# Kernel tuning notes

Measured on AMD Instinct MI355X. Metric: run time of the kernel, lower is better.

Reference implementation:

```python
import jax, jax.numpy as jnp
import numpy as np

N, E, IN, H, L, NB, G = 50000, 300000, 64, 256, 4, 181, 64
EPS = 1e-5
NEG_SLOPE = 0.2


def segment_softmax(e, seg, n):
    m = jax.ops.segment_max(e, seg, num_segments=n)
    a = jnp.exp(e - m[seg])
    d = jax.ops.segment_sum(a, seg, num_segments=n)
    return a / d[seg]


def setup_inputs() -> dict:
    key = jax.random.key(0)
    ks = jax.random.split(key, 32)
    p = lambda k, shape, fan: (jax.random.normal(k, shape, jnp.float32) / np.sqrt(fan)).astype(jnp.float32)
    inp = {}
    inp["x"] = jax.random.normal(ks[0], (N, IN), jnp.float32)
    inp["edge_index"] = jax.random.randint(ks[1], (2, E), 0, N, jnp.int64)
    inp["batch"] = jnp.sort(jax.random.randint(ks[2], (N,), 0, G, jnp.int64))
    inp["W_in"] = p(ks[3], (H, IN), IN); inp["b_in"] = jnp.zeros((H,), jnp.float32)
    inp["Wl"] = p(ks[4], (L, H, H), H); inp["bl"] = jnp.zeros((L, H), jnp.float32)
    inp["Wr"] = p(ks[5], (L, H, H), H); inp["br"] = jnp.zeros((L, H), jnp.float32)
    inp["att"] = p(ks[6], (L, H), H)
    inp["bias_c"] = jnp.zeros((L, H), jnp.float32)
    inp["ln_g"] = jnp.ones((L, H), jnp.float32); inp["ln_b"] = jnp.zeros((L, H), jnp.float32)
    inp["Wg1"] = p(ks[7], (H, H), H); inp["bg1"] = jnp.zeros((H,), jnp.float32)
    inp["Wg2"] = p(ks[8], (1, H), H); inp["bg2"] = jnp.zeros((1,), jnp.float32)
    inp["Ws"] = p(ks[9], (H, H), H); inp["bs"] = jnp.zeros((H,), jnp.float32)
    inp["Wc"] = p(ks[10], (NB, H), H); inp["bc"] = jnp.zeros((NB,), jnp.float32)
    inp["Wr1"] = p(ks[11], (128, H), H); inp["br1"] = jnp.zeros((128,), jnp.float32)
    inp["Wr2"] = p(ks[12], (1, 128), 128); inp["br2"] = jnp.zeros((1,), jnp.float32)
    return inp


def reference(x, edge_index, batch, W_in, b_in, Wl, bl, Wr, br, att, bias_c, ln_g, ln_b,
              Wg1, bg1, Wg2, bg2, Ws, bs, Wc, bc, Wr1, br1, Wr2, br2):
    n = x.shape[0]
    x = x @ W_in.T + b_in  # input projection -> [N,H]
    loops = jnp.arange(n)
    src = jnp.concatenate([edge_index[0], loops])  # GATv2 add_self_loops=True
    dst = jnp.concatenate([edge_index[1], loops])
    for l in range(L):
        x_res = x
        xl = x @ Wl[l].T + bl[l]  # lin_l (source)
        xr = x @ Wr[l].T + br[l]  # lin_r (target)
        h = jax.nn.leaky_relu(xl[src] + xr[dst], NEG_SLOPE)  # [E+N, H]
        e = h @ att[l]                                       # [E+N]
        alpha = segment_softmax(e, dst, n)
        out = jax.ops.segment_sum(alpha[:, None] * xl[src], dst, num_segments=n) + bias_c[l]
        mu = out.mean(-1, keepdims=True)
        var = out.var(-1, keepdims=True)
        out = (out - mu) / jnp.sqrt(var + EPS) * ln_g[l] + ln_b[l]
        x = jax.nn.relu(out) + x_res  # dropout is identity at eval
    gate = jax.nn.relu(x @ Wg1.T + bg1) @ Wg2.T + bg2  # [N,1]
    a = segment_softmax(gate[:, 0], batch, G)
    pooled = jax.ops.segment_sum(a[:, None] * x, batch, num_segments=G)  # [G,H]
    z = jax.nn.relu(pooled @ Ws.T + bs)
    cls_logits = z @ Wc.T + bc                                   # [G,NB]
    residual = jnp.tanh(jax.nn.relu(z @ Wr1.T + br1) @ Wr2.T + br2)[:, 0]  # [G]
    return cls_logits, residual
```

## Files before the change

### kernel.cpp

```cpp
#include <hip/hip_runtime.h>
#include <math.h>

#define N_NODES 50000
#define N_EDGES 300000
#define IN_DIM 64
#define H 256
#define LAYERS 4
#define NB 181
#define NGRAPH 64
#define EE (N_EDGES + N_NODES)
#define NEG_SLOPE 0.2f
#define LN_EPS 1e-5f

typedef unsigned short u16;
typedef __attribute__((ext_vector_type(8))) _Float16 half8;
typedef __attribute__((ext_vector_type(2))) _Float16 half2v;
typedef __attribute__((ext_vector_type(4))) float floatx4;

__device__ __forceinline__ u16 f2h(float f) {
  _Float16 h = (_Float16)f;
  return __builtin_bit_cast(u16, h);
}
__device__ __forceinline__ float h2f(u16 b) {
  return (float)__builtin_bit_cast(_Float16, b);
}

__device__ __forceinline__ float wave_reduce_sum(float v) {
  #pragma unroll
  for (int off = 32; off > 0; off >>= 1) v += __shfl_xor(v, off, 64);
  return v;
}

__global__ void cast_f16_kernel(const float* __restrict__ in, u16* __restrict__ out, int n4) {
  int i = blockIdx.x * 256 + threadIdx.x;
  if (i < n4) {
    float4 f = ((const float4*)in)[i];
    ushort4 o;
    o.x = f2h(f.x); o.y = f2h(f.y); o.z = f2h(f.z); o.w = f2h(f.w);
    ((ushort4*)out)[i] = o;
  }
}

__global__ void cast_weights_kernel(
    const float* __restrict__ W_in, const float* __restrict__ Wg1,
    const float* __restrict__ Wl, const float* __restrict__ Wr,
    u16* __restrict__ win_h, u16* __restrict__ wg1_h,
    u16* __restrict__ wl_h, u16* __restrict__ wr_h)
{
  int i = blockIdx.x * 256 + threadIdx.x;
  int which = blockIdx.y;
  const float* s; u16* dd; int n4;
  if (which == 0)      { s = W_in; dd = win_h; n4 = H * IN_DIM / 4; }
  else if (which == 1) { s = Wg1;  dd = wg1_h; n4 = H * H / 4; }
  else if (which == 2) { s = Wl;   dd = wl_h;  n4 = LAYERS * H * H / 4; }
  else                 { s = Wr;   dd = wr_h;  n4 = LAYERS * H * H / 4; }
  if (i < n4) {
    float4 f = ((const float4*)s)[i];
    ushort4 o;
    o.x = f2h(f.x); o.y = f2h(f.y); o.z = f2h(f.z); o.w = f2h(f.w);
    ((ushort4*)dd)[i] = o;
  }
}

__global__ void init_counts_kernel(int* __restrict__ cnt) {
  int i = blockIdx.x * 256 + threadIdx.x;
  if (i < N_NODES) cnt[i] = 1;
}

__global__ void count_edges_kernel(const int* __restrict__ dst, int* __restrict__ cnt) {
  int e = blockIdx.x * 256 + threadIdx.x;
  if (e < N_EDGES) atomicAdd(&cnt[dst[e]], 1);
}

__global__ void scan_blocks_kernel(const int* __restrict__ cnt, int* __restrict__ partial,
                                   int* __restrict__ bsums, int n) {
  __shared__ int buf[256];
  int tid = threadIdx.x;
  int i = blockIdx.x * 256 + tid;
  buf[tid] = (i < n) ? cnt[i] : 0;
  __syncthreads();
  #pragma unroll
  for (int off = 1; off < 256; off <<= 1) {
    int t = (tid >= off) ? buf[tid - off] : 0;
    __syncthreads();
    buf[tid] += t;
    __syncthreads();
  }
  if (i < n) partial[i] = buf[tid];
  if (tid == 255) bsums[blockIdx.x] = buf[255];
}

__global__ void scan_sums_kernel(int* __restrict__ bsums, int nblk) {
  __shared__ int buf[256];
  int tid = threadIdx.x;
  buf[tid] = (tid < nblk) ? bsums[tid] : 0;
  __syncthreads();
  #pragma unroll
  for (int off = 1; off < 256; off <<= 1) {
    int t = (tid >= off) ? buf[tid - off] : 0;
    __syncthreads();
    buf[tid] += t;
    __syncthreads();
  }
  if (tid < nblk) bsums[tid] = buf[tid];
}

__global__ void scan_write_kernel(const int* __restrict__ partial, const int* __restrict__ bsums,
                                  int* __restrict__ rowp, int n) {
  int i = blockIdx.x * 256 + threadIdx.x;
  if (i < n) {
    int b = blockIdx.x;
    int off = (b > 0) ? bsums[b - 1] : 0;
    rowp[i + 1] = partial[i] + off;
    if (i == 0) rowp[0] = 0;
  }
}

__global__ void fill_self_kernel(const int* __restrict__ rowp, int* __restrict__ col,
                                 int* __restrict__ fillpos) {
  int i = blockIdx.x * 256 + threadIdx.x;
  if (i < N_NODES) {
    int p = rowp[i];
    col[p] = i;
    fillpos[i] = p + 1;
  }
}

__global__ void fill_edges_kernel(const int* __restrict__ src, const int* __restrict__ dst,
                                  int* __restrict__ fillpos, int* __restrict__ col) {
  int e = blockIdx.x * 256 + threadIdx.x;
  if (e < N_EDGES) {
    int d = dst[e];
    int p = atomicAdd(&fillpos[d], 1);
    col[p] = src[e];
  }
}

#define GTM 128
#define GTK 64
#define LDB 72
#define SSTR 132

__global__ __launch_bounds__(256) void gemm_proj_kernel(
    const u16* __restrict__ A, const u16* __restrict__ W,
    const float* __restrict__ bias, u16* __restrict__ outh, int M, int K)
{
  __shared__ u16 smem[2 * GTM * LDB];
  u16* As = smem;
  u16* Bs = smem + GTM * LDB;
  int tid = threadIdx.x;
  int lane = tid & 63;
  int wave = tid >> 6;
  int wm = (wave >> 1) * 64;
  int wn = (wave & 1) * 64;
  int bm = blockIdx.y * GTM;
  int n0 = blockIdx.x * 128;
  int lr = tid >> 3;
  int lc = (tid & 7) * 8;

  floatx4 zero4 = {0.f, 0.f, 0.f, 0.f};
  floatx4 acc[4][4];
  #pragma unroll
  for (int i = 0; i < 4; i++)
    #pragma unroll
    for (int j = 0; j < 4; j++) acc[i][j] = zero4;

  int q8 = (lane >> 4) * 8;
  int mrow = lane & 15;

  for (int k0 = 0; k0 < K; k0 += GTK) {
    __syncthreads();
    #pragma unroll
    for (int p = 0; p < 4; p++) {
      int row = lr + p * 32;
      int gr = bm + row;
      uint4 av = {0, 0, 0, 0};
      if (gr < M) av = *(const uint4*)&A[(size_t)gr * K + k0 + lc];
      *(uint4*)&As[row * LDB + lc] = av;
      uint4 bv = *(const uint4*)&W[(size_t)(n0 + row) * K + k0 + lc];
      *(uint4*)&Bs[row * LDB + lc] = bv;
    }
    __syncthreads();
    #pragma unroll
    for (int h = 0; h < 2; h++) {
      half8 af[4], bf[4];
      #pragma unroll
      for (int i = 0; i < 4; i++)
        af[i] = *(const half8*)&As[(wm + i * 16 + mrow) * LDB + h * 32 + q8];
      #pragma unroll
      for (int j = 0; j < 4; j++)
        bf[j] = *(const half8*)&Bs[(wn + j * 16 + mrow) * LDB + h * 32 + q8];
      #pragma unroll
      for (int i = 0; i < 4; i++)
        #pragma unroll
        for (int j = 0; j < 4; j++)
          acc[i][j] = __builtin_amdgcn_mfma_f32_16x16x32_f16(af[i], bf[j], acc[i][j], 0, 0, 0);
    }
  }

  __syncthreads();
  u16* stage = smem;
  int ccol = lane & 15;
  int crow4 = (lane >> 4) * 4;
  #pragma unroll
  for (int j = 0; j < 4; j++) {
    float bv = bias[n0 + wn + j * 16 + ccol];
    #pragma unroll
    for (int i = 0; i < 4; i++) {
      #pragma unroll
      for (int r = 0; r < 4; r++) {
        int row = wm + i * 16 + crow4 + r;
        stage[row * SSTR + wn + j * 16 + ccol] = f2h(acc[i][j][r] + bv);
      }
    }
  }
  __syncthreads();
  int rr = tid >> 1;
  int c0 = (tid & 1) * 64;
  int grow = bm + rr;
  if (grow < M) {
    const ushort4* sp = (const ushort4*)&stage[rr * SSTR + c0];
    ushort4* gp = (ushort4*)&outh[(size_t)grow * H + n0 + c0];
    #pragma unroll
    for (int q = 0; q < 16; q++) gp[q] = sp[q];
  }
}

#define DTM 64
#define AST 264
#define SSTR2 132

__global__ __launch_bounds__(256) void gemm_dual2_kernel(
    const u16* __restrict__ A, const u16* __restrict__ Wlb, const u16* __restrict__ Wrb,
    const float* __restrict__ biasL, const float* __restrict__ biasR,
    u16* __restrict__ outL, u16* __restrict__ outR, int M)
{
  __shared__ u16 As[DTM * AST];
  __shared__ u16 Bs[128 * LDB];
  int tid = threadIdx.x;
  int lane = tid & 63;
  int wave = tid >> 6;
  int wn = wave * 32;
  int bm = blockIdx.x * DTM;
  int mrow = lane & 15;
  int q8 = (lane >> 4) * 8;
  int ccol = lane & 15;
  int crow4 = (lane >> 4) * 4;

  {
    int col = (tid & 31) * 8;
    int r0 = tid >> 5;
    #pragma unroll
    for (int it = 0; it < 8; it++) {
      int row = r0 + it * 8;
      int gr = bm + row;
      uint4 av = {0, 0, 0, 0};
      if (gr < M) av = *(const uint4*)&A[(size_t)gr * H + col];
      *(uint4*)&As[row * AST + col] = av;
    }
  }

  floatx4 zero4 = {0.f, 0.f, 0.f, 0.f};

  for (int nt = 0; nt < 4; nt++) {
    const u16* W = (nt < 2) ? Wlb : Wrb;
    const float* bias = (nt < 2) ? biasL : biasR;
    u16* outp = (nt < 2) ? outL : outR;
    int n0 = (nt & 1) * 128;

    floatx4 acc[4][2];
    #pragma unroll
    for (int i = 0; i < 4; i++) {
      acc[i][0] = zero4;
      acc[i][1] = zero4;
    }

    for (int k0 = 0; k0 < H; k0 += 64) {
      __syncthreads();
      {
        int col = (tid & 7) * 8;
        int r0 = tid >> 3;
        #pragma unroll
        for (int p2 = 0; p2 < 4; p2++) {
          int row = r0 + p2 * 32;
          uint4 bv = *(const uint4*)&W[(size_t)(n0 + row) * H + k0 + col];
          *(uint4*)&Bs[row * LDB + col] = bv;
        }
      }
      __syncthreads();
      #pragma unroll
      for (int h = 0; h < 2; h++) {
        half8 af[4], bf[2];
        #pragma unroll
        for (int i = 0; i < 4; i++)
          af[i] = *(const half8*)&As[(i * 16 + mrow) * AST + k0 + h * 32 + q8];
        #pragma unroll
        for (int j = 0; j < 2; j++)
          bf[j] = *(const half8*)&Bs[(wn + j * 16 + mrow) * LDB + h * 32 + q8];
        #pragma unroll
        for (int i = 0; i < 4; i++)
          #pragma unroll
          for (int j = 0; j < 2; j++)
            acc[i][j] = __builtin_amdgcn_mfma_f32_16x16x32_f16(af[i], bf[j], acc[i][j], 0, 0, 0);
      }
    }

    __syncthreads();
    u16* stage = Bs;
    #pragma unroll
    for (int j = 0; j < 2; j++) {
      float bv = bias[n0 + wn + j * 16 + ccol];
      #pragma unroll
      for (int i = 0; i < 4; i++) {
        #pragma unroll
        for (int r = 0; r < 4; r++) {
          int row = i * 16 + crow4 + r;
          stage[row * SSTR2 + wn + j * 16 + ccol] = f2h(acc[i][j][r] + bv);
        }
      }
    }
    __syncthreads();
    {
      int row = tid >> 2;
      int c0 = (tid & 3) * 32;
      int grow = bm + row;
      if (grow < M) {
        #pragma unroll
        for (int q = 0; q < 8; q++)
          *(ushort4*)&outp[(size_t)grow * H + n0 + c0 + q * 4] =
              *(const ushort4*)&stage[row * SSTR2 + c0 + q * 4];
      }
    }
  }
}

__global__ __launch_bounds__(256) void gemm_gate_kernel(
    const u16* __restrict__ A, const u16* __restrict__ W,
    const float* __restrict__ bias, const float* __restrict__ Wg2,
    float* __restrict__ gate, int M)
{
  __shared__ u16 smem[2 * GTM * LDB];
  u16* As = smem;
  u16* Bs = smem + GTM * LDB;
  int tid = threadIdx.x;
  int lane = tid & 63;
  int wave = tid >> 6;
  int wm = (wave >> 1) * 64;
  int wn = (wave & 1) * 64;
  int bm = blockIdx.y * GTM;
  int bn = blockIdx.x * 128;
  int lr = tid >> 3;
  int lc = (tid & 7) * 8;

  floatx4 zero4 = {0.f, 0.f, 0.f, 0.f};
  floatx4 acc[4][4];
  #pragma unroll
  for (int i = 0; i < 4; i++)
    #pragma unroll
    for (int j = 0; j < 4; j++) acc[i][j] = zero4;

  int q8 = (lane >> 4) * 8;
  int mrow = lane & 15;

  for (int k0 = 0; k0 < H; k0 += GTK) {
    __syncthreads();
    #pragma unroll
    for (int p = 0; p < 4; p++) {
      int row = lr + p * 32;
      int gr = bm + row;
      uint4 av = {0, 0, 0, 0};
      if (gr < M) av = *(const uint4*)&A[(size_t)gr * H + k0 + lc];
      *(uint4*)&As[row * LDB + lc] = av;
      uint4 bv = *(const uint4*)&W[(size_t)(bn + row) * H + k0 + lc];
      *(uint4*)&Bs[row * LDB + lc] = bv;
    }
    __syncthreads();
    #pragma unroll
    for (int h = 0; h < 2; h++) {
      half8 af[4], bf[4];
      #pragma unroll
      for (int i = 0; i < 4; i++)
        af[i] = *(const half8*)&As[(wm + i * 16 + mrow) * LDB + h * 32 + q8];
      #pragma unroll
      for (int j = 0; j < 4; j++)
        bf[j] = *(const half8*)&Bs[(wn + j * 16 + mrow) * LDB + h * 32 + q8];
      #pragma unroll
      for (int i = 0; i < 4; i++)
        #pragma unroll
        for (int j = 0; j < 4; j++)
          acc[i][j] = __builtin_amdgcn_mfma_f32_16x16x32_f16(af[i], bf[j], acc[i][j], 0, 0, 0);
    }
  }

  int ccol = lane & 15;
  float bv[4], wv[4];
  #pragma unroll
  for (int j = 0; j < 4; j++) {
    int col = bn + wn + j * 16 + ccol;
    bv[j] = bias[col];
    wv[j] = Wg2[col];
  }
  #pragma unroll
  for (int i = 0; i < 4; i++) {
    #pragma unroll
    for (int r = 0; r < 4; r++) {
      float p = 0.f;
      #pragma unroll
      for (int j = 0; j < 4; j++) {
        float hcol = fmaxf(acc[i][j][r] + bv[j], 0.f);
        p += hcol * wv[j];
      }
      p += __shfl_xor(p, 1, 64);
      p += __shfl_xor(p, 2, 64);
      p += __shfl_xor(p, 4, 64);
      p += __shfl_xor(p, 8, 64);
      int row = bm + wm + i * 16 + (lane >> 4) * 4 + r;
      if ((lane & 15) == 0 && row < M) atomicAdd(&gate[row], p);
    }
  }
}

__global__ __launch_bounds__(256) void layer_fused_kernel(
    const u16* __restrict__ xl, const u16* __restrict__ xr,
    u16* __restrict__ xst,
    const int* __restrict__ rowp, const int* __restrict__ col,
    const float* __restrict__ att, const float* __restrict__ bias_c,
    const float* __restrict__ ln_g, const float* __restrict__ ln_b)
{
  int lane = threadIdx.x & 63;
  int v = blockIdx.x * 4 + (threadIdx.x >> 6);
  if (v >= N_NODES) return;
  int f4 = lane << 2;
  size_t rowbase = (size_t)v * H;

  uint2 xrq = *(const uint2*)&xr[rowbase + f4];
  half2v xrh[2] = {__builtin_bit_cast(half2v, xrq.x), __builtin_bit_cast(half2v, xrq.y)};
  float4 attv = *(const float4*)&att[f4];
  half2v ath[2] = {{(_Float16)attv.x, (_Float16)attv.y},
                   {(_Float16)attv.z, (_Float16)attv.w}};
  const half2v kslope = {(_Float16)NEG_SLOPE, (_Float16)NEG_SLOPE};

  int beg = rowp[v], end = rowp[v + 1];
  float m = -INFINITY, d = 0.f;
  half2v o0 = {(_Float16)0.f, (_Float16)0.f};
  half2v o1 = {(_Float16)0.f, (_Float16)0.f};

  for (int p = beg; p < end; p += 2) {
    int valid1 = (p + 1 < end);
    int u0 = col[p];
    int u1 = valid1 ? col[p + 1] : u0;
    uint2 aq0 = *(const uint2*)&xl[(size_t)u0 * H + f4];
    uint2 aq1 = *(const uint2*)&xl[(size_t)u1 * H + f4];
    half2v a00 = __builtin_bit_cast(half2v, aq0.x);
    half2v a01 = __builtin_bit_cast(half2v, aq0.y);
    half2v a10 = __builtin_bit_cast(half2v, aq1.x);
    half2v a11 = __builtin_bit_cast(half2v, aq1.y);
    half2v h00 = a00 + xrh[0], h01 = a01 + xrh[1];
    half2v h10 = a10 + xrh[0], h11 = a11 + xrh[1];
    half2v l00 = __builtin_elementwise_max(h00, h00 * kslope);
    half2v l01 = __builtin_elementwise_max(h01, h01 * kslope);
    half2v l10 = __builtin_elementwise_max(h10, h10 * kslope);
    half2v l11 = __builtin_elementwise_max(h11, h11 * kslope);
#if __has_builtin(__builtin_amdgcn_fdot2)
    float pe0 = __builtin_amdgcn_fdot2(l01, ath[1],
                 __builtin_amdgcn_fdot2(l00, ath[0], 0.f, false), false);
    float pe1 = __builtin_amdgcn_fdot2(l11, ath[1],
                 __builtin_amdgcn_fdot2(l10, ath[0], 0.f, false), false);
#else
    float pe0 = (float)l00[0] * (float)ath[0][0] + (float)l00[1] * (float)ath[0][1]
              + (float)l01[0] * (float)ath[1][0] + (float)l01[1] * (float)ath[1][1];
    float pe1 = (float)l10[0] * (float)ath[0][0] + (float)l10[1] * (float)ath[0][1]
              + (float)l11[0] * (float)ath[1][0] + (float)l11[1] * (float)ath[1][1];
#endif
    #pragma unroll
    for (int off = 32; off > 0; off >>= 1) {
      pe0 += __shfl_xor(pe0, off, 64);
      pe1 += __shfl_xor(pe1, off, 64);
    }
    if (!valid1) pe1 = -INFINITY;
    float mn = fmaxf(m, fmaxf(pe0, pe1));
    float sc = __expf(m - mn);
    float w0 = __expf(pe0 - mn);
    float w1 = __expf(pe1 - mn);
    d = fmaf(d, sc, w0 + w1);
    _Float16 sch = (_Float16)sc, w0h = (_Float16)w0, w1h = (_Float16)w1;
    half2v scp = {sch, sch}, w0p = {w0h, w0h}, w1p = {w1h, w1h};
    half2v t0 = a00 * w0p + a10 * w1p;
    half2v t1 = a01 * w0p + a11 * w1p;
    o0 = o0 * scp + t0;
    o1 = o1 * scp + t1;
    m = mn;
  }

  float invd = 1.0f / d;
  float4 bc4 = *(const float4*)&bias_c[f4];
  float ox = fmaf((float)o0[0], invd, bc4.x);
  float oy = fmaf((float)o0[1], invd, bc4.y);
  float oz = fmaf((float)o1[0], invd, bc4.z);
  float ow = fmaf((float)o1[1], invd, bc4.w);
  float s = wave_reduce_sum(ox + oy + oz + ow);
  float mean = s * (1.0f / H);
  float cx = ox - mean, cy = oy - mean, cz = oz - mean, cw = ow - mean;
  float sq = wave_reduce_sum(cx * cx + cy * cy + cz * cz + cw * cw);
  float rstd = rsqrtf(sq * (1.0f / H) + LN_EPS);
  float4 g4 = *(const float4*)&ln_g[f4];
  float4 b4 = *(const float4*)&ln_b[f4];
  uint2 resq = *(const uint2*)&xst[rowbase + f4];
  half2v r0 = __builtin_bit_cast(half2v, resq.x);
  half2v r1 = __builtin_bit_cast(half2v, resq.y);
  float yx = fmaxf(fmaf(cx * rstd, g4.x, b4.x), 0.f) + (float)r0[0];
  float yy = fmaxf(fmaf(cy * rstd, g4.y, b4.y), 0.f) + (float)r0[1];
  float yz = fmaxf(fmaf(cz * rstd, g4.z, b4.z), 0.f) + (float)r1[0];
  float yw = fmaxf(fmaf(cw * rstd, g4.w, b4.w), 0.f) + (float)r1[1];
  ushort4 yb;
  yb.x = f2h(yx); yb.y = f2h(yy); yb.z = f2h(yz); yb.w = f2h(yw);
  *(ushort4*)&xst[rowbase + f4] = yb;
}

__global__ void gate_init_kernel(float* __restrict__ gate, const float* __restrict__ bg2,
                                 int* __restrict__ gstart, int* __restrict__ gend) {
  int i = blockIdx.x * 256 + threadIdx.x;
  if (i < N_NODES) gate[i] = bg2[0];
  if (i < NGRAPH) { gstart[i] = 0; gend[i] = 0; }
}

__global__ void gbounds_kernel(const int* __restrict__ batch, int* __restrict__ gstart,
                               int* __restrict__ gend) {
  int i = blockIdx.x * 256 + threadIdx.x;
  if (i < N_NODES) {
    int b = batch[i];
    if (i == 0 || batch[i - 1] != b) gstart[b] = i;
    if (i == N_NODES - 1 || batch[i + 1] != b) gend[b] = i + 1;
  }
}

__global__ __launch_bounds__(256) void pool_prep_kernel(
    const float* __restrict__ gate, const int* __restrict__ gstart,
    const int* __restrict__ gend, float* __restrict__ gmax, float* __restrict__ gdinv,
    float* __restrict__ pooled)
{
  __shared__ float red[256];
  int g = blockIdx.x, tid = threadIdx.x;
  pooled[(size_t)g * H + tid] = 0.f;
  int s = gstart[g], e = gend[g];
  float lm = -INFINITY;
  for (int i = s + tid; i < e; i += 256) lm = fmaxf(lm, gate[i]);
  red[tid] = lm;
  __syncthreads();
  for (int off = 128; off; off >>= 1) {
    if (tid < off) red[tid] = fmaxf(red[tid], red[tid + off]);
    __syncthreads();
  }
  float m = red[0];
  __syncthreads();
  float lsum = 0.0f;
  for (int i = s + tid; i < e; i += 256) lsum += __expf(gate[i] - m);
  red[tid] = lsum;
  __syncthreads();
  for (int off = 128; off; off >>= 1) {
    if (tid < off) red[tid] += red[tid + off];
    __syncthreads();
  }
  if (tid == 0) {
    gmax[g] = m;
    gdinv[g] = (s < e) ? 1.0f / red[0] : 0.0f;
  }
}

__global__ __launch_bounds__(256) void pool_accum_kernel(
    const float* __restrict__ gate, const u16* __restrict__ xh,
    const int* __restrict__ batch, const float* __restrict__ gmax,
    const float* __restrict__ gdinv, float* __restrict__ pooled)
{
  __shared__ float wl[128];
  __shared__ int gl[128];
  int b0 = blockIdx.x * 128;
  int tid = threadIdx.x;
  if (tid < 128) {
    int v = b0 + tid;
    if (v < N_NODES) {
      int g = batch[v];
      gl[tid] = g;
      wl[tid] = __expf(gate[v] - gmax[g]) * gdinv[g];
    } else {
      gl[tid] = -1;
      wl[tid] = 0.f;
    }
  }
  __syncthreads();
  int cnt = min(128, N_NODES - b0);
  float acc = 0.f;
  int cur = gl[0];
  for (int j = 0; j < cnt; j++) {
    int g = gl[j];
    if (g != cur) {
      atomicAdd(&pooled[(size_t)cur * H + tid], acc);
      acc = 0.f;
      cur = g;
    }
    acc += wl[j] * h2f(xh[(size_t)(b0 + j) * H + tid]);
  }
  if (cur >= 0) atomicAdd(&pooled[(size_t)cur * H + tid], acc);
}

__global__ __launch_bounds__(256) void head_kernel(
    const float* __restrict__ pooled,
    const float* __restrict__ Ws, const float* __restrict__ bs,
    const float* __restrict__ Wc, const float* __restrict__ bc,
    const float* __restrict__ Wr1, const float* __restrict__ br1,
    const float* __restrict__ Wr2, const float* __restrict__ br2,
    float* __restrict__ out)
{
  __shared__ float psh[256];
  __shared__ float zsh[256];
  __shared__ float r1sh[128];
  int g = blockIdx.x, tid = threadIdx.x;
  psh[tid] = pooled[(size_t)g * H + tid];
  __syncthreads();
  {
    float acc = bs[tid];
    const float4* wr = (const float4*)&Ws[(size_t)tid * H];
    for (int k4 = 0; k4 < H / 4; k4++) {
      float4 wv = wr[k4];
      float4 av = *(const float4*)&psh[k4 * 4];
      acc += av.x * wv.x + av.y * wv.y + av.z * wv.z + av.w * wv.w;
    }
    zsh[tid] = fmaxf(acc, 0.f);
  }
  __syncthreads();
  if (tid < NB) {
    float acc = bc[tid];
    const float4* wr = (const float4*)&Wc[(size_t)tid * H];
    for (int k4 = 0; k4 < H / 4; k4++) {
      float4 wv = wr[k4];
      float4 av = *(const float4*)&zsh[k4 * 4];
      acc += av.x * wv.x + av.y * wv.y + av.z * wv.z + av.w * wv.w;
    }
    out[(size_t)g * NB + tid] = acc;
  }
  if (tid < 128) {
    float acc = br1[tid];
    const float4* wr = (const float4*)&Wr1[(size_t)tid * H];
    for (int k4 = 0; k4 < H / 4; k4++) {
      float4 wv = wr[k4];
      float4 av = *(const float4*)&zsh[k4 * 4];
      acc += av.x * wv.x + av.y * wv.y + av.z * wv.z + av.w * wv.w;
    }
    r1sh[tid] = fmaxf(acc, 0.f);
  }
  __syncthreads();
  if (tid < 64) {
    float s2 = r1sh[tid] * Wr2[tid] + r1sh[tid + 64] * Wr2[tid + 64];
    s2 = wave_reduce_sum(s2);
    if (tid == 0) out[(size_t)NGRAPH * NB + g] = tanhf(s2 + br2[0]);
  }
}

extern "C" void kernel_launch(void* const* d_in, const int* in_sizes, int n_in,
                              void* d_out, int out_size, void* d_ws, size_t ws_size,
                              hipStream_t stream) {
  const float* x_in   = (const float*)d_in[0];
  const int*   eidx   = (const int*)d_in[1];
  const int*   batch  = (const int*)d_in[2];
  const float* W_in   = (const float*)d_in[3];
  const float* b_in   = (const float*)d_in[4];
  const float* Wl     = (const float*)d_in[5];
  const float* bl     = (const float*)d_in[6];
  const float* Wr     = (const float*)d_in[7];
  const float* br     = (const float*)d_in[8];
  const float* att    = (const float*)d_in[9];
  const float* bias_c = (const float*)d_in[10];
  const float* ln_g   = (const float*)d_in[11];
  const float* ln_b   = (const float*)d_in[12];
  const float* Wg1    = (const float*)d_in[13];
  const float* bg1    = (const float*)d_in[14];
  const float* Wg2    = (const float*)d_in[15];
  const float* bg2    = (const float*)d_in[16];
  const float* Ws     = (const float*)d_in[17];
  const float* bs     = (const float*)d_in[18];
  const float* Wc     = (const float*)d_in[19];
  const float* bc     = (const float*)d_in[20];
  const float* Wr1    = (const float*)d_in[21];
  const float* br1    = (const float*)d_in[22];
  const float* Wr2    = (const float*)d_in[23];
  const float* br2    = (const float*)d_in[24];
  float* out = (float*)d_out;

  char* w = (char*)d_ws;
  u16* x_h    = (u16*)w;    w += sizeof(u16) * (size_t)N_NODES * H;
  u16* xl_h   = (u16*)w;    w += sizeof(u16) * (size_t)N_NODES * H;
  u16* xr_h   = (u16*)w;    w += sizeof(u16) * (size_t)N_NODES * H;
  u16* xin_h  = (u16*)w;    w += sizeof(u16) * (size_t)N_NODES * IN_DIM;
  u16* win_h  = (u16*)w;    w += sizeof(u16) * (size_t)H * IN_DIM;
  u16* wl_h   = (u16*)w;    w += sizeof(u16) * (size_t)LAYERS * H * H;
  u16* wr_h   = (u16*)w;    w += sizeof(u16) * (size_t)LAYERS * H * H;
  u16* wg1_h  = (u16*)w;    w += sizeof(u16) * (size_t)H * H;
  float* pooled = (float*)w; w += sizeof(float) * NGRAPH * H;
  float* gate = (float*)w;  w += sizeof(float) * N_NODES;
  float* gmax = (float*)w;  w += sizeof(float) * NGRAPH;
  float* gdinv= (float*)w;  w += sizeof(float) * NGRAPH;
  int* cnt    = (int*)w;    w += sizeof(int) * N_NODES;
  int* rowp   = (int*)w;    w += sizeof(int) * (N_NODES + 1);
  int* col    = (int*)w;    w += sizeof(int) * EE;
  int* partial= (int*)w;    w += sizeof(int) * N_NODES;
  int* bsums  = (int*)w;    w += sizeof(int) * 256;
  int* gstart = (int*)w;    w += sizeof(int) * NGRAPH;
  int* gend   = (int*)w;    w += sizeof(int) * NGRAPH;
  (void)ws_size; (void)n_in; (void)in_sizes; (void)out_size;

  const int* src = eidx;
  const int* dst = eidx + N_EDGES;
  int nblkN = (N_NODES + 255) / 256;
  int nblkE = (N_EDGES + 255) / 256;
  int mtiles = (N_NODES + GTM - 1) / GTM;
  int mtiles2 = (N_NODES + DTM - 1) / DTM;

  init_counts_kernel<<<nblkN, 256, 0, stream>>>(cnt);
  count_edges_kernel<<<nblkE, 256, 0, stream>>>(dst, cnt);
  scan_blocks_kernel<<<nblkN, 256, 0, stream>>>(cnt, partial, bsums, N_NODES);
  scan_sums_kernel<<<1, 256, 0, stream>>>(bsums, nblkN);
  scan_write_kernel<<<nblkN, 256, 0, stream>>>(partial, bsums, rowp, N_NODES);
  fill_self_kernel<<<nblkN, 256, 0, stream>>>(rowp, col, cnt);
  fill_edges_kernel<<<nblkE, 256, 0, stream>>>(src, dst, cnt, col);

  {
    int maxn4 = LAYERS * H * H / 4;
    dim3 gcast((maxn4 + 255) / 256, 4);
    cast_weights_kernel<<<gcast, 256, 0, stream>>>(W_in, Wg1, Wl, Wr,
                                                   win_h, wg1_h, wl_h, wr_h);
    int n4 = N_NODES * IN_DIM / 4;
    cast_f16_kernel<<<(n4 + 255) / 256, 256, 0, stream>>>(x_in, xin_h, n4);
  }

  dim3 gproj(2, mtiles);
  gemm_proj_kernel<<<gproj, 256, 0, stream>>>(xin_h, win_h, b_in, x_h, N_NODES, IN_DIM);

  int nblkV = N_NODES / 4;
  for (int l = 0; l < LAYERS; l++) {
    gemm_dual2_kernel<<<mtiles2, 256, 0, stream>>>(x_h,
        wl_h + (size_t)l * H * H, wr_h + (size_t)l * H * H,
        bl + l * H, br + l * H, xl_h, xr_h, N_NODES);
    layer_fused_kernel<<<nblkV, 256, 0, stream>>>(xl_h, xr_h, x_h, rowp, col,
        att + l * H, bias_c + l * H, ln_g + l * H, ln_b + l * H);
  }

  gate_init_kernel<<<nblkN, 256, 0, stream>>>(gate, bg2, gstart, gend);
  dim3 ggate(2, mtiles);
  gemm_gate_kernel<<<ggate, 256, 0, stream>>>(x_h, wg1_h, bg1, Wg2, gate, N_NODES);

  gbounds_kernel<<<nblkN, 256, 0, stream>>>(batch, gstart, gend);
  pool_prep_kernel<<<NGRAPH, 256, 0, stream>>>(gate, gstart, gend, gmax, gdinv, pooled);
  pool_accum_kernel<<<(N_NODES + 127) / 128, 256, 0, stream>>>(gate, x_h, batch, gmax, gdinv, pooled);

  head_kernel<<<NGRAPH, 256, 0, stream>>>(pooled, Ws, bs, Wc, bc, Wr1, br1, Wr2, br2, out);
}
```

Before: 651.1 us.

## Split GATv2 layer into edge-parallel score kernel and node aggregation kernel

```diff
diff --git a/kernel.cpp b/kernel.cpp
--- a/kernel.cpp
+++ b/kernel.cpp
@@ -44,8 +44,10 @@
 __global__ void cast_weights_kernel(
     const float* __restrict__ W_in, const float* __restrict__ Wg1,
     const float* __restrict__ Wl, const float* __restrict__ Wr,
+    const float* __restrict__ att,
     u16* __restrict__ win_h, u16* __restrict__ wg1_h,
-    u16* __restrict__ wl_h, u16* __restrict__ wr_h)
+    u16* __restrict__ wl_h, u16* __restrict__ wr_h,
+    u16* __restrict__ att_h)
 {
   int i = blockIdx.x * 256 + threadIdx.x;
   int which = blockIdx.y;
@@ -53,7 +55,8 @@
   if (which == 0)      { s = W_in; dd = win_h; n4 = H * IN_DIM / 4; }
   else if (which == 1) { s = Wg1;  dd = wg1_h; n4 = H * H / 4; }
   else if (which == 2) { s = Wl;   dd = wl_h;  n4 = LAYERS * H * H / 4; }
-  else                 { s = Wr;   dd = wr_h;  n4 = LAYERS * H * H / 4; }
+  else if (which == 3) { s = Wr;   dd = wr_h;  n4 = LAYERS * H * H / 4; }
+  else                 { s = att;  dd = att_h; n4 = LAYERS * H / 4; }
   if (i < n4) {
     float4 f = ((const float4*)s)[i];
     ushort4 o;
@@ -117,22 +120,25 @@
 }
 
 __global__ void fill_self_kernel(const int* __restrict__ rowp, int* __restrict__ col,
-                                 int* __restrict__ fillpos) {
+                                 int* __restrict__ rowdst, int* __restrict__ fillpos) {
   int i = blockIdx.x * 256 + threadIdx.x;
   if (i < N_NODES) {
     int p = rowp[i];
     col[p] = i;
+    rowdst[p] = i;
     fillpos[i] = p + 1;
   }
 }
 
 __global__ void fill_edges_kernel(const int* __restrict__ src, const int* __restrict__ dst,
-                                  int* __restrict__ fillpos, int* __restrict__ col) {
+                                  int* __restrict__ fillpos, int* __restrict__ col,
+                                  int* __restrict__ rowdst) {
   int e = blockIdx.x * 256 + threadIdx.x;
   if (e < N_EDGES) {
     int d = dst[e];
     int p = atomicAdd(&fillpos[d], 1);
     col[p] = src[e];
+    rowdst[p] = d;
   }
 }
 
@@ -420,11 +426,58 @@
   }
 }
 
-__global__ __launch_bounds__(256) void layer_fused_kernel(
+__global__ __launch_bounds__(256) void edge_score_kernel(
     const u16* __restrict__ xl, const u16* __restrict__ xr,
-    u16* __restrict__ xst,
+    const u16* __restrict__ att_h,
+    const int* __restrict__ col, const int* __restrict__ rowdst,
+    float* __restrict__ e_w)
+{
+  int tid = threadIdx.x;
+  int lane = tid & 63;
+  int wave = tid >> 6;
+  int q = lane & 3;
+  int ei = lane >> 2;
+  int p = blockIdx.x * 64 + wave * 16 + ei;
+  if (p >= EE) return;
+  int u = col[p];
+  int v = rowdst[p];
+  const u16* xlrow = xl + (size_t)u * H + q * 64;
+  const u16* xrrow = xr + (size_t)v * H + q * 64;
+  const u16* at = att_h + q * 64;
+  const half2v kslope = {(_Float16)NEG_SLOPE, (_Float16)NEG_SLOPE};
+  float pe = 0.f;
+  #pragma unroll
+  for (int i = 0; i < 8; i++) {
+    uint4 aq = *(const uint4*)&xlrow[i * 8];
+    uint4 bq = *(const uint4*)&xrrow[i * 8];
+    uint4 tq = *(const uint4*)&at[i * 8];
+    unsigned int ap[4] = {aq.x, aq.y, aq.z, aq.w};
+    unsigned int bp[4] = {bq.x, bq.y, bq.z, bq.w};
+    unsigned int tp[4] = {tq.x, tq.y, tq.z, tq.w};
+    #pragma unroll
+    for (int c = 0; c < 4; c++) {
+      half2v a = __builtin_bit_cast(half2v, ap[c]);
+      half2v b = __builtin_bit_cast(half2v, bp[c]);
+      half2v t = __builtin_bit_cast(half2v, tp[c]);
+      half2v h = a + b;
+      half2v l = __builtin_elementwise_max(h, h * kslope);
+#if __has_builtin(__builtin_amdgcn_fdot2)
+      pe = __builtin_amdgcn_fdot2(l, t, pe, false);
+#else
+      pe += (float)l[0] * (float)t[0] + (float)l[1] * (float)t[1];
+#endif
+    }
+  }
+  pe += __shfl_xor(pe, 1, 64);
+  pe += __shfl_xor(pe, 2, 64);
+  if (q == 0) e_w[p] = pe;
+}
+
+__global__ __launch_bounds__(256) void layer_agg_kernel(
+    const u16* __restrict__ xl, u16* __restrict__ xst,
     const int* __restrict__ rowp, const int* __restrict__ col,
-    const float* __restrict__ att, const float* __restrict__ bias_c,
+    const float* __restrict__ e_w,
+    const float* __restrict__ bias_c,
     const float* __restrict__ ln_g, const float* __restrict__ ln_b)
 {
   int lane = threadIdx.x & 63;
@@ -432,72 +485,55 @@
   if (v >= N_NODES) return;
   int f4 = lane << 2;
   size_t rowbase = (size_t)v * H;
-
-  uint2 xrq = *(const uint2*)&xr[rowbase + f4];
-  half2v xrh[2] = {__builtin_bit_cast(half2v, xrq.x), __builtin_bit_cast(half2v, xrq.y)};
-  float4 attv = *(const float4*)&att[f4];
-  half2v ath[2] = {{(_Float16)attv.x, (_Float16)attv.y},
-                   {(_Float16)attv.z, (_Float16)attv.w}};
-  const half2v kslope = {(_Float16)NEG_SLOPE, (_Float16)NEG_SLOPE};
-
   int beg = rowp[v], end = rowp[v + 1];
-  float m = -INFINITY, d = 0.f;
-  half2v o0 = {(_Float16)0.f, (_Float16)0.f};
-  half2v o1 = {(_Float16)0.f, (_Float16)0.f};
-
-  for (int p = beg; p < end; p += 2) {
-    int valid1 = (p + 1 < end);
-    int u0 = col[p];
-    int u1 = valid1 ? col[p + 1] : u0;
-    uint2 aq0 = *(const uint2*)&xl[(size_t)u0 * H + f4];
-    uint2 aq1 = *(const uint2*)&xl[(size_t)u1 * H + f4];
-    half2v a00 = __builtin_bit_cast(half2v, aq0.x);
-    half2v a01 = __builtin_bit_cast(half2v, aq0.y);
-    half2v a10 = __builtin_bit_cast(half2v, aq1.x);
-    half2v a11 = __builtin_bit_cast(half2v, aq1.y);
-    half2v h00 = a00 + xrh[0], h01 = a01 + xrh[1];
-    half2v h10 = a10 + xrh[0], h11 = a11 + xrh[1];
-    half2v l00 = __builtin_elementwise_max(h00, h00 * kslope);
-    half2v l01 = __builtin_elementwise_max(h01, h01 * kslope);
-    half2v l10 = __builtin_elementwise_max(h10, h10 * kslope);
-    half2v l11 = __builtin_elementwise_max(h11, h11 * kslope);
-#if __has_builtin(__builtin_amdgcn_fdot2)
-    float pe0 = __builtin_amdgcn_fdot2(l01, ath[1],
-                 __builtin_amdgcn_fdot2(l00, ath[0], 0.f, false), false);
-    float pe1 = __builtin_amdgcn_fdot2(l11, ath[1],
-                 __builtin_amdgcn_fdot2(l10, ath[0], 0.f, false), false);
-#else
-    float pe0 = (float)l00[0] * (float)ath[0][0] + (float)l00[1] * (float)ath[0][1]
-              + (float)l01[0] * (float)ath[1][0] + (float)l01[1] * (float)ath[1][1];
-    float pe1 = (float)l10[0] * (float)ath[0][0] + (float)l10[1] * (float)ath[0][1]
-              + (float)l11[0] * (float)ath[1][0] + (float)l11[1] * (float)ath[1][1];
-#endif
-    #pragma unroll
-    for (int off = 32; off > 0; off >>= 1) {
-      pe0 += __shfl_xor(pe0, off, 64);
-      pe1 += __shfl_xor(pe1, off, 64);
-    }
-    if (!valid1) pe1 = -INFINITY;
-    float mn = fmaxf(m, fmaxf(pe0, pe1));
-    float sc = __expf(m - mn);
-    float w0 = __expf(pe0 - mn);
-    float w1 = __expf(pe1 - mn);
-    d = fmaf(d, sc, w0 + w1);
-    _Float16 sch = (_Float16)sc, w0h = (_Float16)w0, w1h = (_Float16)w1;
-    half2v scp = {sch, sch}, w0p = {w0h, w0h}, w1p = {w1h, w1h};
-    half2v t0 = a00 * w0p + a10 * w1p;
-    half2v t1 = a01 * w0p + a11 * w1p;
-    o0 = o0 * scp + t0;
-    o1 = o1 * scp + t1;
-    m = mn;
-  }
-
+  int deg = end - beg;
+
+  float lm = -INFINITY;
+  for (int j = lane; j < deg; j += 64) lm = fmaxf(lm, e_w[beg + j]);
+  #pragma unroll
+  for (int off = 32; off > 0; off >>= 1) lm = fmaxf(lm, __shfl_xor(lm, off, 64));
+  float m = lm;
+  float wreg = 0.f;
+  int colreg = 0;
+  float lsum = 0.f;
+  for (int j = lane; j < deg; j += 64) {
+    float wj = __expf(e_w[beg + j] - m);
+    if (j < 64) { wreg = wj; colreg = col[beg + j]; }
+    lsum += wj;
+  }
+  float d = wave_reduce_sum(lsum);
   float invd = 1.0f / d;
+
+  float o0 = 0.f, o1 = 0.f, o2 = 0.f, o3 = 0.f;
+  int jmax = min(deg, 64);
+  for (int j = 0; j < jmax; j++) {
+    float wgt = __shfl(wreg, j, 64);
+    int u = __shfl(colreg, j, 64);
+    uint2 aq = *(const uint2*)&xl[(size_t)u * H + f4];
+    half2v a0 = __builtin_bit_cast(half2v, aq.x);
+    half2v a1 = __builtin_bit_cast(half2v, aq.y);
+    o0 = fmaf(wgt, (float)a0[0], o0);
+    o1 = fmaf(wgt, (float)a0[1], o1);
+    o2 = fmaf(wgt, (float)a1[0], o2);
+    o3 = fmaf(wgt, (float)a1[1], o3);
+  }
+  for (int j = 64; j < deg; j++) {
+    float wgt = __expf(e_w[beg + j] - m);
+    int u = col[beg + j];
+    uint2 aq = *(const uint2*)&xl[(size_t)u * H + f4];
+    half2v a0 = __builtin_bit_cast(half2v, aq.x);
+    half2v a1 = __builtin_bit_cast(half2v, aq.y);
+    o0 = fmaf(wgt, (float)a0[0], o0);
+    o1 = fmaf(wgt, (float)a0[1], o1);
+    o2 = fmaf(wgt, (float)a1[0], o2);
+    o3 = fmaf(wgt, (float)a1[1], o3);
+  }
+
   float4 bc4 = *(const float4*)&bias_c[f4];
-  float ox = fmaf((float)o0[0], invd, bc4.x);
-  float oy = fmaf((float)o0[1], invd, bc4.y);
-  float oz = fmaf((float)o1[0], invd, bc4.z);
-  float ow = fmaf((float)o1[1], invd, bc4.w);
+  float ox = fmaf(o0, invd, bc4.x);
+  float oy = fmaf(o1, invd, bc4.y);
+  float oz = fmaf(o2, invd, bc4.z);
+  float ow = fmaf(o3, invd, bc4.w);
   float s = wave_reduce_sum(ox + oy + oz + ow);
   float mean = s * (1.0f / H);
   float cx = ox - mean, cy = oy - mean, cz = oz - mean, cw = ow - mean;
@@ -695,6 +731,8 @@
   u16* wl_h   = (u16*)w;    w += sizeof(u16) * (size_t)LAYERS * H * H;
   u16* wr_h   = (u16*)w;    w += sizeof(u16) * (size_t)LAYERS * H * H;
   u16* wg1_h  = (u16*)w;    w += sizeof(u16) * (size_t)H * H;
+  u16* att_h  = (u16*)w;    w += sizeof(u16) * (size_t)LAYERS * H;
+  float* e_w  = (float*)w;  w += sizeof(float) * EE;
   float* pooled = (float*)w; w += sizeof(float) * NGRAPH * H;
   float* gate = (float*)w;  w += sizeof(float) * N_NODES;
   float* gmax = (float*)w;  w += sizeof(float) * NGRAPH;
@@ -702,6 +740,7 @@
   int* cnt    = (int*)w;    w += sizeof(int) * N_NODES;
   int* rowp   = (int*)w;    w += sizeof(int) * (N_NODES + 1);
   int* col    = (int*)w;    w += sizeof(int) * EE;
+  int* rowdst = (int*)w;    w += sizeof(int) * EE;
   int* partial= (int*)w;    w += sizeof(int) * N_NODES;
   int* bsums  = (int*)w;    w += sizeof(int) * 256;
   int* gstart = (int*)w;    w += sizeof(int) * NGRAPH;
@@ -714,20 +753,21 @@
   int nblkE = (N_EDGES + 255) / 256;
   int mtiles = (N_NODES + GTM - 1) / GTM;
   int mtiles2 = (N_NODES + DTM - 1) / DTM;
+  int sblk = (EE + 63) / 64;
 
   init_counts_kernel<<<nblkN, 256, 0, stream>>>(cnt);
   count_edges_kernel<<<nblkE, 256, 0, stream>>>(dst, cnt);
   scan_blocks_kernel<<<nblkN, 256, 0, stream>>>(cnt, partial, bsums, N_NODES);
   scan_sums_kernel<<<1, 256, 0, stream>>>(bsums, nblkN);
   scan_write_kernel<<<nblkN, 256, 0, stream>>>(partial, bsums, rowp, N_NODES);
-  fill_self_kernel<<<nblkN, 256, 0, stream>>>(rowp, col, cnt);
-  fill_edges_kernel<<<nblkE, 256, 0, stream>>>(src, dst, cnt, col);
+  fill_self_kernel<<<nblkN, 256, 0, stream>>>(rowp, col, rowdst, cnt);
+  fill_edges_kernel<<<nblkE, 256, 0, stream>>>(src, dst, cnt, col, rowdst);
 
   {
     int maxn4 = LAYERS * H * H / 4;
-    dim3 gcast((maxn4 + 255) / 256, 4);
-    cast_weights_kernel<<<gcast, 256, 0, stream>>>(W_in, Wg1, Wl, Wr,
-                                                   win_h, wg1_h, wl_h, wr_h);
+    dim3 gcast((maxn4 + 255) / 256, 5);
+    cast_weights_kernel<<<gcast, 256, 0, stream>>>(W_in, Wg1, Wl, Wr, att,
+                                                   win_h, wg1_h, wl_h, wr_h, att_h);
     int n4 = N_NODES * IN_DIM / 4;
     cast_f16_kernel<<<(n4 + 255) / 256, 256, 0, stream>>>(x_in, xin_h, n4);
   }
@@ -740,8 +780,10 @@
     gemm_dual2_kernel<<<mtiles2, 256, 0, stream>>>(x_h,
         wl_h + (size_t)l * H * H, wr_h + (size_t)l * H * H,
         bl + l * H, br + l * H, xl_h, xr_h, N_NODES);
-    layer_fused_kernel<<<nblkV, 256, 0, stream>>>(xl_h, xr_h, x_h, rowp, col,
-        att + l * H, bias_c + l * H, ln_g + l * H, ln_b + l * H);
+    edge_score_kernel<<<sblk, 256, 0, stream>>>(xl_h, xr_h, att_h + l * H,
+        col, rowdst, e_w);
+    layer_agg_kernel<<<nblkV, 256, 0, stream>>>(xl_h, x_h, rowp, col, e_w,
+        bias_c + l * H, ln_g + l * H, ln_b + l * H);
   }
 
   gate_init_kernel<<<nblkN, 256, 0, stream>>>(gate, bg2, gstart, gend);
```

After: 860.4 us. 1.32x slower.
